# Performance work log

Measured on AMD Instinct MI355X. Metric: run time of the kernel, lower is better.

The kernel has to match this reference:

```python
import jax, jax.numpy as jnp
import numpy as np

B, L, D_MODEL = 4, 2048, 1024
N_HEADS, FEAT, HEAD_DIM = 16, 16, 64
CHUNK = 128
EPS = 1e-12


def taylor_exp(x):
    """2nd-order Taylor feature map of exp(q.k/sqrt(d)).
    x: (b, h, l, f) -> (b, h, l, 1 + f + f*f)"""
    f = x.shape[-1]
    r2 = jnp.sqrt(jnp.asarray(2.0, x.dtype))
    rd = jnp.sqrt(jnp.asarray(float(f), x.dtype))      # sqrt(d)
    rrd = jnp.sqrt(rd)                                  # d**0.25
    x2 = (x[..., :, None] * x[..., None, :]).reshape(*x.shape[:-1], f * f) / r2
    ones = jnp.ones_like(x[..., :1])
    return jnp.concatenate([ones, x / rrd, x2 / rd], axis=-1)


def setup_inputs() -> dict:
    key = jax.random.key(0)
    k1, k2, k3, k4, k5 = jax.random.split(key, 5)
    s = 0.02
    return {
        "hidden_states": jax.random.normal(k1, (B, L, D_MODEL), jnp.float32),
        "Wq": jax.random.normal(k2, (N_HEADS * FEAT, D_MODEL), jnp.float32) * s,
        "Wk": jax.random.normal(k3, (N_HEADS * FEAT, D_MODEL), jnp.float32) * s,
        "Wv": jax.random.normal(k4, (N_HEADS * HEAD_DIM, D_MODEL), jnp.float32) * s,
        "Wo": jax.random.normal(k5, (D_MODEL, N_HEADS * HEAD_DIM), jnp.float32) * s,
    }


def reference(hidden_states, Wq, Wk, Wv, Wo):
    b, l, _ = hidden_states.shape
    # projections (Linear without bias: x @ W.T)
    q = (hidden_states @ Wq.T).reshape(b, l, N_HEADS, FEAT).transpose(0, 2, 1, 3)
    k = (hidden_states @ Wk.T).reshape(b, l, N_HEADS, FEAT).transpose(0, 2, 1, 3)
    v = (hidden_states @ Wv.T).reshape(b, l, N_HEADS, HEAD_DIM).transpose(0, 2, 1, 3)

    qf = taylor_exp(q)  # (b, h, l, De) with De = 1 + f + f^2 = 273
    kf = taylor_exp(k)
    De = qf.shape[-1]

    # chunked causal linear attention: same math as cumulative kv-state
    n = l // CHUNK
    qc = jnp.moveaxis(qf.reshape(b, N_HEADS, n, CHUNK, De), 2, 0)       # (n,b,h,c,De)
    kc = jnp.moveaxis(kf.reshape(b, N_HEADS, n, CHUNK, De), 2, 0)
    vc = jnp.moveaxis(v.reshape(b, N_HEADS, n, CHUNK, HEAD_DIM), 2, 0)
    mask = jnp.tril(jnp.ones((CHUNK, CHUNK), qf.dtype))

    def step(carry, xs):
        S, z = carry                       # S: (b,h,De,e), z: (b,h,De)
        qi, ki, vi = xs
        attn = jnp.einsum('bhid,bhjd->bhij', qi, ki) * mask
        num = jnp.einsum('bhij,bhje->bhie', attn, vi) \
            + jnp.einsum('bhid,bhde->bhie', qi, S)
        den = attn.sum(-1) + jnp.einsum('bhid,bhd->bhi', qi, z)
        yi = num / (den[..., None] + EPS)
        S = S + jnp.einsum('bhjd,bhje->bhde', ki, vi)
        z = z + ki.sum(2)
        return (S, z), yi

    S0 = jnp.zeros((b, N_HEADS, De, HEAD_DIM), qf.dtype)
    z0 = jnp.zeros((b, N_HEADS, De), qf.dtype)
    _, ys = jax.lax.scan(step, (S0, z0), (qc, kc, vc))
    y = jnp.moveaxis(ys, 0, 2).reshape(b, N_HEADS, l, HEAD_DIM)          # (b,h,l,e)
    y = y.transpose(0, 2, 1, 3).reshape(b, l, N_HEADS * HEAD_DIM)        # (b,l,h*e)
    return y @ Wo.T
```

## Files before the change

kernel.cpp:

```cpp
#include <hip/hip_runtime.h>
#include <hip/hip_bf16.h>

#define BB 4
#define LL 2048
#define DM 1024
#define NH 16
#define FEAT 16
#define HD 64
#define CHUNK 128
#define NCHUNK 16
#define NEXT 65
#define SROW 18720
#define EPS 1e-12f
#define INV_R2RD 0.17677669529663688f
#define QKVLD 1536

typedef short bf16x8_t __attribute__((ext_vector_type(8)));
typedef float f32x4_t  __attribute__((ext_vector_type(4)));

__device__ __forceinline__ float b2f(unsigned short u) {
    union { unsigned int i; float f; } x; x.i = ((unsigned int)u) << 16; return x.f;
}
__device__ __forceinline__ unsigned short f2b(float f) {
    __hip_bfloat16 h = __float2bfloat16(f);
    return *reinterpret_cast<unsigned short*>(&h);
}

__global__ __launch_bounds__(256)
void cast_all(const float* __restrict__ hs, const float* __restrict__ wq,
              const float* __restrict__ wk, const float* __restrict__ wv,
              const float* __restrict__ wo, unsigned short* __restrict__ hs_bf,
              unsigned short* __restrict__ wqkv, unsigned short* __restrict__ wo_bf)
{
    const int i = (blockIdx.x * 256 + threadIdx.x) * 4;
    const float* s; unsigned short* d;
    if (i < 8388608)       { s = hs + i;             d = hs_bf + i; }
    else if (i < 8650752)  { s = wq + (i - 8388608); d = wqkv + (i - 8388608); }
    else if (i < 8912896)  { s = wk + (i - 8650752); d = wqkv + 262144 + (i - 8650752); }
    else if (i < 9961472)  { s = wv + (i - 8912896); d = wqkv + 524288 + (i - 8912896); }
    else if (i < 11010048) { s = wo + (i - 9961472); d = wo_bf + (i - 9961472); }
    else return;
    float4 v = *(const float4*)s;
    ushort4 o; o.x = f2b(v.x); o.y = f2b(v.y); o.z = f2b(v.z); o.w = f2b(v.w);
    *(ushort4*)d = o;
}

__global__ __launch_bounds__(512, 2)
void gemm_bf16_192(const unsigned short* __restrict__ A, const unsigned short* __restrict__ Bw,
                   unsigned short* __restrict__ C, int K, int lda, int ldb, int ldc)
{
    __shared__ unsigned short lds[57344];
    const int tid  = threadIdx.x;
    const int wid  = tid >> 6, lane = tid & 63;
    const int wm   = wid >> 2, wn = wid & 3;
    const int ml   = lane & 15, quad = lane >> 4;
    const int nwg = gridDim.x * gridDim.y;
    const int lin = blockIdx.y * gridDim.x + blockIdx.x;
    const int swz_id = (lin & 7) * (nwg >> 3) + (lin >> 3);
    const int m0   = (swz_id / gridDim.x) * 256, n0 = (swz_id % gridDim.x) * 192;
    const int NT   = K >> 6;

    const int srow  = tid >> 3;
    const int scol  = ((tid & 7) ^ (srow & 7)) << 3;
    const int wbase = wid << 9;

    auto stage_unit = [&](int t, int isB, int u) {
        const unsigned short* g0 = isB ? Bw : A;
        const int ld = isB ? ldb : lda;
        const int rb = (isB ? n0 : m0) + u * 64 + srow;
        unsigned short* lb = lds + (isB ? 32768 + (t & 1) * 12288 : ((t & 1) << 14))
                             + (u << 12) + wbase;
        const unsigned short* g = g0 + (size_t)rb * ld + (t << 6) + scol;
        __builtin_amdgcn_global_load_lds((const __attribute__((address_space(1))) void*)g,
                                         (__attribute__((address_space(3))) void*)lb, 16, 0, 0);
    };

    f32x4_t acc[8][3];
#pragma unroll
    for (int i = 0; i < 8; ++i)
#pragma unroll
        for (int j = 0; j < 3; ++j) acc[i][j] = (f32x4_t){0.f, 0.f, 0.f, 0.f};

    stage_unit(0, 0, 0); stage_unit(0, 0, 1); stage_unit(0, 0, 2); stage_unit(0, 0, 3);
    stage_unit(0, 1, 0); stage_unit(0, 1, 1); stage_unit(0, 1, 2);
    stage_unit(1, 0, 0); stage_unit(1, 0, 1);
    stage_unit(1, 1, 0); stage_unit(1, 1, 1);
    stage_unit(1, 0, 2); stage_unit(1, 0, 3);
    asm volatile("s_waitcnt vmcnt(6)" ::: "memory");
    __builtin_amdgcn_s_barrier();

    const int swz  = (ml & 7) << 3;
    const int c0   = (quad << 3) ^ swz;
    const int c1   = (32 + (quad << 3)) ^ swz;
    const int arow = ml << 6;

    bf16x8_t aA[4][2], bLo[2][2], bN2[2];

    for (int t = 0; t < NT; ++t) {
        const int ab = (t & 1) << 14;
        const int bb = 32768 + (t & 1) * 12288;

#pragma unroll
        for (int m = 0; m < 4; ++m) {
            const int r = ab + ((2 * m + wm) << 10) + arow;
            aA[m][0] = *(const bf16x8_t*)&lds[r + c0];
            aA[m][1] = *(const bf16x8_t*)&lds[r + c1];
        }
#pragma unroll
        for (int n = 0; n < 2; ++n) {
            const int r = bb + (wn * 48 + n * 16 + ml) * 64;
            bLo[n][0] = *(const bf16x8_t*)&lds[r + c0];
            bLo[n][1] = *(const bf16x8_t*)&lds[r + c1];
        }
        if (t + 1 < NT) stage_unit(t + 1, 1, 2);
        __builtin_amdgcn_s_barrier();
        asm volatile("s_waitcnt lgkmcnt(0)" ::: "memory");
        __builtin_amdgcn_sched_barrier(0);
        __builtin_amdgcn_s_setprio(1);
#pragma unroll
        for (int m = 0; m < 4; ++m)
#pragma unroll
            for (int n = 0; n < 2; ++n) {
                acc[m][n] = __builtin_amdgcn_mfma_f32_16x16x32_bf16(aA[m][0], bLo[n][0], acc[m][n], 0, 0, 0);
                acc[m][n] = __builtin_amdgcn_mfma_f32_16x16x32_bf16(aA[m][1], bLo[n][1], acc[m][n], 0, 0, 0);
            }
        __builtin_amdgcn_s_setprio(0);
        __builtin_amdgcn_s_barrier();

        {
            const int r = bb + (wn * 48 + 32 + ml) * 64;
            bN2[0] = *(const bf16x8_t*)&lds[r + c0];
            bN2[1] = *(const bf16x8_t*)&lds[r + c1];
        }
        if (t + 2 < NT) { stage_unit(t + 2, 0, 0); stage_unit(t + 2, 0, 1); }
        __builtin_amdgcn_s_barrier();
        asm volatile("s_waitcnt lgkmcnt(0)" ::: "memory");
        __builtin_amdgcn_sched_barrier(0);
        __builtin_amdgcn_s_setprio(1);
#pragma unroll
        for (int m = 0; m < 4; ++m) {
            acc[m][2] = __builtin_amdgcn_mfma_f32_16x16x32_bf16(aA[m][0], bN2[0], acc[m][2], 0, 0, 0);
            acc[m][2] = __builtin_amdgcn_mfma_f32_16x16x32_bf16(aA[m][1], bN2[1], acc[m][2], 0, 0, 0);
        }
        __builtin_amdgcn_s_setprio(0);
        __builtin_amdgcn_s_barrier();

#pragma unroll
        for (int m = 0; m < 4; ++m) {
            const int r = ab + ((2 * (m + 4) + wm) << 10) + arow;
            aA[m][0] = *(const bf16x8_t*)&lds[r + c0];
            aA[m][1] = *(const bf16x8_t*)&lds[r + c1];
        }
        if (t + 2 < NT) { stage_unit(t + 2, 1, 0); stage_unit(t + 2, 1, 1); }
        __builtin_amdgcn_s_barrier();
        asm volatile("s_waitcnt lgkmcnt(0)" ::: "memory");
        __builtin_amdgcn_sched_barrier(0);
        __builtin_amdgcn_s_setprio(1);
#pragma unroll
        for (int m = 0; m < 4; ++m)
#pragma unroll
            for (int n = 0; n < 2; ++n) {
                acc[4 + m][n] = __builtin_amdgcn_mfma_f32_16x16x32_bf16(aA[m][0], bLo[n][0], acc[4 + m][n], 0, 0, 0);
                acc[4 + m][n] = __builtin_amdgcn_mfma_f32_16x16x32_bf16(aA[m][1], bLo[n][1], acc[4 + m][n], 0, 0, 0);
            }
        __builtin_amdgcn_s_setprio(0);
        __builtin_amdgcn_s_barrier();

        if (t + 2 < NT) { stage_unit(t + 2, 0, 2); stage_unit(t + 2, 0, 3); }
        __builtin_amdgcn_s_barrier();
        asm volatile("s_waitcnt lgkmcnt(0)" ::: "memory");
        __builtin_amdgcn_sched_barrier(0);
        __builtin_amdgcn_s_setprio(1);
#pragma unroll
        for (int m = 0; m < 4; ++m) {
            acc[4 + m][2] = __builtin_amdgcn_mfma_f32_16x16x32_bf16(aA[m][0], bN2[0], acc[4 + m][2], 0, 0, 0);
            acc[4 + m][2] = __builtin_amdgcn_mfma_f32_16x16x32_bf16(aA[m][1], bN2[1], acc[4 + m][2], 0, 0, 0);
        }
        __builtin_amdgcn_s_setprio(0);
        if (t + 2 < NT)      asm volatile("s_waitcnt vmcnt(6)" ::: "memory");
        else if (t + 1 < NT) asm volatile("s_waitcnt vmcnt(0)" ::: "memory");
        __builtin_amdgcn_s_barrier();
    }

#pragma unroll
    for (int m = 0; m < 8; ++m) {
        const int rbase = m0 + (2 * m + wm) * 16 + quad * 4;
#pragma unroll
        for (int n = 0; n < 3; ++n) {
            const int col = n0 + wn * 48 + n * 16 + ml;
#pragma unroll
            for (int r = 0; r < 4; ++r)
                C[(size_t)(rbase + r) * ldc + col] = f2b(acc[m][n][r]);
        }
    }
}

__global__ __launch_bounds__(512, 2)
void gemm_bf16_128x256(const unsigned short* __restrict__ A, const unsigned short* __restrict__ Bw,
                       float* __restrict__ C, int K, int lda, int ldb, int ldc)
{
    __shared__ unsigned short lds[49152];
    const int tid  = threadIdx.x;
    const int wid  = tid >> 6, lane = tid & 63;
    const int wm   = wid >> 2, wn = wid & 3;
    const int ml   = lane & 15, quad = lane >> 4;
    const int nwg = gridDim.x * gridDim.y;
    const int lin = blockIdx.y * gridDim.x + blockIdx.x;
    const int swz_id = (lin & 7) * (nwg >> 3) + (lin >> 3);
    const int m0   = (swz_id / gridDim.x) * 128, n0 = (swz_id % gridDim.x) * 256;
    const int NT   = K >> 6;

    const int srow  = tid >> 3;
    const int scol  = ((tid & 7) ^ (srow & 7)) << 3;
    const int wbase = wid << 9;

    auto stage_unit = [&](int t, int isB, int u) {
        const unsigned short* g0 = isB ? Bw : A;
        const int ld = isB ? ldb : lda;
        const int rb = (isB ? n0 : m0) + u * 64 + srow;
        const int k0 = t << 6;
        unsigned short* lb = lds + (isB ? 16384 : 0) + ((t & 1) << (isB ? 14 : 13))
                             + (u << 12) + wbase;
        const unsigned short* g = g0 + (size_t)rb * ld + k0 + scol;
        __builtin_amdgcn_global_load_lds((const __attribute__((address_space(1))) void*)g,
                                         (__attribute__((address_space(3))) void*)lb, 16, 0, 0);
    };

    f32x4_t acc[4][4];
#pragma unroll
    for (int i = 0; i < 4; ++i)
#pragma unroll
        for (int j = 0; j < 4; ++j) acc[i][j] = (f32x4_t){0.f, 0.f, 0.f, 0.f};

    stage_unit(0, 0, 0); stage_unit(0, 0, 1);
    stage_unit(0, 1, 0); stage_unit(0, 1, 1); stage_unit(0, 1, 2); stage_unit(0, 1, 3);
    stage_unit(1, 0, 0); stage_unit(1, 0, 1);
    stage_unit(1, 1, 0); stage_unit(1, 1, 1);
    asm volatile("s_waitcnt vmcnt(4)" ::: "memory");
    __builtin_amdgcn_s_barrier();

    const int swz  = (ml & 7) << 3;
    const int c0   = (quad << 3) ^ swz;
    const int c1   = (32 + (quad << 3)) ^ swz;
    const int arow = ml << 6;

    bf16x8_t aA[4][2], bF[2][2];

    for (int t = 0; t < NT; ++t) {
        const int ab = (t & 1) << 13;
        const int bb = 16384 + ((t & 1) << 14);

#pragma unroll
        for (int m = 0; m < 4; ++m) {
            const int r = ab + ((2 * m + wm) << 10) + arow;
            aA[m][0] = *(const bf16x8_t*)&lds[r + c0];
            aA[m][1] = *(const bf16x8_t*)&lds[r + c1];
        }
#pragma unroll
        for (int n = 0; n < 2; ++n) {
            const int r = bb + ((4 * n + wn) << 10) + arow;
            bF[n][0] = *(const bf16x8_t*)&lds[r + c0];
            bF[n][1] = *(const bf16x8_t*)&lds[r + c1];
        }
        if (t + 1 < NT) { stage_unit(t + 1, 1, 2); stage_unit(t + 1, 1, 3); }
        __builtin_amdgcn_s_barrier();
        asm volatile("s_waitcnt lgkmcnt(0)" ::: "memory");
        __builtin_amdgcn_sched_barrier(0);
        __builtin_amdgcn_s_setprio(1);
#pragma unroll
        for (int m = 0; m < 4; ++m)
#pragma unroll
            for (int n = 0; n < 2; ++n) {
                acc[m][n] = __builtin_amdgcn_mfma_f32_16x16x32_bf16(aA[m][0], bF[n][0], acc[m][n], 0, 0, 0);
                acc[m][n] = __builtin_amdgcn_mfma_f32_16x16x32_bf16(aA[m][1], bF[n][1], acc[m][n], 0, 0, 0);
            }
        __builtin_amdgcn_s_setprio(0);
        __builtin_amdgcn_s_barrier();

#pragma unroll
        for (int n = 0; n < 2; ++n) {
            const int r = bb + ((4 * (n + 2) + wn) << 10) + arow;
            bF[n][0] = *(const bf16x8_t*)&lds[r + c0];
            bF[n][1] = *(const bf16x8_t*)&lds[r + c1];
        }
        if (t + 2 < NT) {
            stage_unit(t + 2, 0, 0); stage_unit(t + 2, 0, 1);
            stage_unit(t + 2, 1, 0); stage_unit(t + 2, 1, 1);
        }
        __builtin_amdgcn_s_barrier();
        asm volatile("s_waitcnt lgkmcnt(0)" ::: "memory");
        __builtin_amdgcn_sched_barrier(0);
        __builtin_amdgcn_s_setprio(1);
#pragma unroll
        for (int m = 0; m < 4; ++m)
#pragma unroll
            for (int n = 0; n < 2; ++n) {
                acc[m][2 + n] = __builtin_amdgcn_mfma_f32_16x16x32_bf16(aA[m][0], bF[n][0], acc[m][2 + n], 0, 0, 0);
                acc[m][2 + n] = __builtin_amdgcn_mfma_f32_16x16x32_bf16(aA[m][1], bF[n][1], acc[m][2 + n], 0, 0, 0);
            }
        __builtin_amdgcn_s_setprio(0);
        if (t + 2 < NT)      asm volatile("s_waitcnt vmcnt(4)" ::: "memory");
        else if (t + 1 < NT) asm volatile("s_waitcnt vmcnt(0)" ::: "memory");
        __builtin_amdgcn_s_barrier();
    }

#pragma unroll
    for (int m = 0; m < 4; ++m) {
        const int rbase = m0 + (2 * m + wm) * 16 + quad * 4;
#pragma unroll
        for (int n = 0; n < 4; ++n) {
            const int col = n0 + (4 * n + wn) * 16 + ml;
#pragma unroll
            for (int r = 0; r < 4; ++r)
                C[(size_t)(rbase + r) * ldc + col] = acc[m][n][r];
        }
    }
}

__global__ __launch_bounds__(256)
void state_scan(const unsigned short* __restrict__ qkv, unsigned short* __restrict__ STg)
{
    __shared__ unsigned short KT[16 * 136];
    __shared__ unsigned short VT[80 * 136];

    const int g  = blockIdx.x & 3, bh = blockIdx.x >> 2;
    const int b = bh >> 4, h = bh & 15;
    const int tid = threadIdx.x;
    const int wave = tid >> 6, lane = tid & 63;
    const int ml = lane & 15, kg8 = (lane >> 4) * 8, quad4 = (lane >> 4) * 4;
    const int mtA = g + 4 * wave;
    const bool hasB = (wave == 0) && (g < 2);
    const int mtB = 16 + g;

    const int row = tid >> 1, half = tid & 1;
    const unsigned short* src = qkv + (size_t)(b * LL) * QKVLD;

    if (half == 0) {
        VT[64 * 136 + row] = 0x3F80;
    } else {
#pragma unroll
        for (int e = 65; e < 80; ++e) VT[e * 136 + row] = 0;
    }

    uint4 kvn, vvn[4];
    {
        const size_t rg = (size_t)row * QKVLD;
        kvn = *(const uint4*)(src + rg + 256 + h * 16 + half * 8);
#pragma unroll
        for (int cc = 0; cc < 4; ++cc)
            vvn[cc] = *(const uint4*)(src + rg + 512 + h * 64 + half * 32 + cc * 8);
    }

    f32x4_t prefA[5], prefB[5];
#pragma unroll
    for (int nt = 0; nt < 5; ++nt) {
        prefA[nt] = (f32x4_t){0.f, 0.f, 0.f, 0.f};
        prefB[nt] = (f32x4_t){0.f, 0.f, 0.f, 0.f};
    }

    auto do_tile = [&](int mt, f32x4_t* pref, size_t Sb) {
        const int d = mt * 16 + ml;
        bf16x8_t af[4];
#pragma unroll
        for (int ks = 0; ks < 4; ++ks) {
            const int jb = ks * 32 + kg8;
            unsigned short o[8];
            if (d >= 24 && d < 280) {
                const int e = d - 24, a = e >> 4, bq = e & 15;
                bf16x8_t ka = *(const bf16x8_t*)&KT[a  * 136 + jb];
                bf16x8_t kb = *(const bf16x8_t*)&KT[bq * 136 + jb];
#pragma unroll
                for (int j = 0; j < 8; ++j)
                    o[j] = f2b(b2f((unsigned short)ka[j]) * b2f((unsigned short)kb[j]) * INV_R2RD);
            } else if (d == 0) {
#pragma unroll
                for (int j = 0; j < 8; ++j) o[j] = 0x3F80;
            } else if (d <= 16) {
                bf16x8_t kx = *(const bf16x8_t*)&KT[(d - 1) * 136 + jb];
#pragma unroll
                for (int j = 0; j < 8; ++j) o[j] = f2b(b2f((unsigned short)kx[j]) * 0.5f);
            } else {
#pragma unroll
                for (int j = 0; j < 8; ++j) o[j] = 0;
            }
            af[ks] = *(const bf16x8_t*)o;
        }
        bf16x8_t bfr[5][4];
#pragma unroll
        for (int nt = 0; nt < 5; ++nt)
#pragma unroll
            for (int ks = 0; ks < 4; ++ks)
                bfr[nt][ks] = *(const bf16x8_t*)&VT[(nt * 16 + ml) * 136 + ks * 32 + kg8];
#pragma unroll
        for (int nt = 0; nt < 5; ++nt) {
            ushort4 pk;
            pk.x = f2b(pref[nt][0]); pk.y = f2b(pref[nt][1]);
            pk.z = f2b(pref[nt][2]); pk.w = f2b(pref[nt][3]);
            if (nt < 4) {
                *(ushort4*)(STg + Sb + (size_t)mt * 1040 + (nt * 16 + ml) * 16 + quad4) = pk;
            } else if (ml == 0) {
                *(ushort4*)(STg + Sb + (size_t)mt * 1040 + 1024 + quad4) = pk;
            }
        }
        __builtin_amdgcn_s_setprio(1);
#pragma unroll
        for (int nt = 0; nt < 5; ++nt)
#pragma unroll
            for (int ks = 0; ks < 4; ++ks)
                pref[nt] = __builtin_amdgcn_mfma_f32_16x16x32_bf16(af[ks], bfr[nt][ks], pref[nt], 0, 0, 0);
        __builtin_amdgcn_s_setprio(0);
    };

    for (int c = 0; c < NCHUNK; ++c) {
        {
            const unsigned short* kp = (const unsigned short*)&kvn;
#pragma unroll
            for (int i = 0; i < 8; ++i) KT[(half * 8 + i) * 136 + row] = kp[i];
#pragma unroll
            for (int cc = 0; cc < 4; ++cc) {
                const unsigned short* vp = (const unsigned short*)&vvn[cc];
#pragma unroll
                for (int i = 0; i < 8; ++i) VT[(half * 32 + cc * 8 + i) * 136 + row] = vp[i];
            }
        }
        __syncthreads();
        if (c + 1 < NCHUNK) {
            const size_t rg = (size_t)((c + 1) * CHUNK + row) * QKVLD;
            kvn = *(const uint4*)(src + rg + 256 + h * 16 + half * 8);
#pragma unroll
            for (int cc = 0; cc < 4; ++cc)
                vvn[cc] = *(const uint4*)(src + rg + 512 + h * 64 + half * 32 + cc * 8);
        }

        const size_t Sb = (size_t)(bh * NCHUNK + c) * SROW;
        do_tile(mtA, prefA, Sb);
        if (hasB) do_tile(mtB, prefB, Sb);
        __syncthreads();
    }
}

#define OFF_VT 0
#define OFF_QP 0
#define OFF_KP 5120
#define OFF_A  10880

__global__ __launch_bounds__(256)
void out_kernel(const unsigned short* __restrict__ qkv_ro, const unsigned short* __restrict__ STg,
                unsigned short* __restrict__ qkv_w)
{
    __shared__ unsigned short smem[28288];

    const int x = blockIdx.x;
    const int c = x & 15, bh = x >> 4;
    const int b = bh >> 4, h = bh & 15;
    const int tid = threadIdx.x;
    const int w = tid >> 6, lane = tid & 63;
    const int ml = lane & 15, quad = lane >> 4, kg8 = quad * 8;
    const size_t rowbase = (size_t)(b * LL + c * CHUNK);
    const size_t Sbase = (size_t)x * SROW;

    const unsigned short* stp = STg + Sbase + (size_t)(quad >> 1) * 1040 + (quad & 1) * 8;
    bf16x8_t stf[3][5];
    auto ldst = [&](int kq, int slot) {
#pragma unroll
        for (int nt = 0; nt < 5; ++nt)
            stf[slot][nt] = *(const bf16x8_t*)(stp + (size_t)kq * 2080 + (nt * 16 + ml) * 16);
    };

    const int row = tid >> 1, half = tid & 1;
    uint4 qv = *(const uint4*)(qkv_ro + (rowbase + row) * QKVLD + h * 16 + half * 8);
    uint4 kv = *(const uint4*)(qkv_ro + (rowbase + row) * QKVLD + 256 + h * 16 + half * 8);
    uint4 vreg[4];
#pragma unroll
    for (int cc = 0; cc < 4; ++cc)
        vreg[cc] = *(const uint4*)(qkv_ro + (rowbase + row) * QKVLD + 512 + h * 64 + half * 32 + cc * 8);
    ldst(0, 0);
    ldst(1, 1);

    *(uint4*)&smem[OFF_QP + row * 40 + half * 8] = qv;
    *(uint4*)&smem[OFF_QP + row * 40 + 16 + half * 8] = (uint4){0, 0, 0, 0};
    *(uint4*)&smem[OFF_KP + row * 40 + half * 8] = kv;
    *(uint4*)&smem[OFF_KP + row * 40 + 16 + half * 8] = (uint4){0, 0, 0, 0};
    __syncthreads();

    {
        bf16x8_t q0 = *(const bf16x8_t*)&smem[OFF_QP + (w * 32 + ml) * 40 + kg8];
        bf16x8_t q1 = *(const bf16x8_t*)&smem[OFF_QP + (w * 32 + 16 + ml) * 40 + kg8];
#pragma unroll
        for (int nt = 0; nt < 8; ++nt) {
            bf16x8_t kf = *(const bf16x8_t*)&smem[OFF_KP + (nt * 16 + ml) * 40 + kg8];
            f32x4_t a0 = __builtin_amdgcn_mfma_f32_16x16x32_bf16(q0, kf, (f32x4_t){0,0,0,0}, 0, 0, 0);
            f32x4_t a1 = __builtin_amdgcn_mfma_f32_16x16x32_bf16(q1, kf, (f32x4_t){0,0,0,0}, 0, 0, 0);
            const int j = nt * 16 + ml;
#pragma unroll
            for (int r = 0; r < 4; ++r) {
                int i0 = w * 32 + quad * 4 + r;
                float s0 = a0[r] * 0.25f;
                float v0 = (j <= i0) ? (1.f + s0 + 0.5f * s0 * s0) : 0.f;
                smem[OFF_A + i0 * 136 + j] = f2b(v0);
                int i1 = i0 + 16;
                float s1 = a1[r] * 0.25f;
                float v1 = (j <= i1) ? (1.f + s1 + 0.5f * s1 * s1) : 0.f;
                smem[OFF_A + i1 * 136 + j] = f2b(v1);
            }
        }
    }
    const int r0 = w * 32 + ml, r1 = r0 + 16;
    float qA[16], qB[16];
    {
        bf16x8_t t0 = *(const bf16x8_t*)&smem[OFF_QP + r0 * 40];
        bf16x8_t t1 = *(const bf16x8_t*)&smem[OFF_QP + r0 * 40 + 8];
        bf16x8_t t2 = *(const bf16x8_t*)&smem[OFF_QP + r1 * 40];
        bf16x8_t t3 = *(const bf16x8_t*)&smem[OFF_QP + r1 * 40 + 8];
#pragma unroll
        for (int i = 0; i < 8; ++i) {
            qA[i] = b2f((unsigned short)t0[i]); qA[8 + i] = b2f((unsigned short)t1[i]);
            qB[i] = b2f((unsigned short)t2[i]); qB[8 + i] = b2f((unsigned short)t3[i]);
        }
    }
    float qselA[8], qselB[8];
#pragma unroll
    for (int j = 0; j < 8; ++j) {
        qselA[j] = (quad & 1) ? qA[j] : qA[8 + j];
        qselB[j] = (quad & 1) ? qB[j] : qB[8 + j];
    }
    __syncthreads();

    {
#pragma unroll
        for (int cc = 0; cc < 4; ++cc) {
            const unsigned short* vp = (const unsigned short*)&vreg[cc];
#pragma unroll
            for (int i = 0; i < 8; ++i) smem[OFF_VT + (half * 32 + cc * 8 + i) * 136 + row] = vp[i];
        }
        if (half == 0) {
            smem[OFF_VT + 64 * 136 + row] = 0x3F80;
        } else {
#pragma unroll
            for (int e = 65; e < 80; ++e) smem[OFF_VT + e * 136 + row] = 0;
        }
    }
    __syncthreads();

    f32x4_t acc[2][5];
#pragma unroll
    for (int mt = 0; mt < 2; ++mt)
#pragma unroll
        for (int nt = 0; nt < 5; ++nt) acc[mt][nt] = (f32x4_t){0.f, 0.f, 0.f, 0.f};

    ldst(2, 2);

#pragma unroll
    for (int ks = 0; ks < 4; ++ks) {
        bf16x8_t af0 = *(const bf16x8_t*)&smem[OFF_A + (w * 32 + ml) * 136 + ks * 32 + kg8];
        bf16x8_t af1 = *(const bf16x8_t*)&smem[OFF_A + (w * 32 + 16 + ml) * 136 + ks * 32 + kg8];
        __builtin_amdgcn_s_setprio(1);
#pragma unroll
        for (int nt = 0; nt < 5; ++nt) {
            bf16x8_t bv = *(const bf16x8_t*)&smem[OFF_VT + (nt * 16 + ml) * 136 + ks * 32 + kg8];
            acc[0][nt] = __builtin_amdgcn_mfma_f32_16x16x32_bf16(af0, bv, acc[0][nt], 0, 0, 0);
            acc[1][nt] = __builtin_amdgcn_mfma_f32_16x16x32_bf16(af1, bv, acc[1][nt], 0, 0, 0);
        }
        __builtin_amdgcn_s_setprio(0);
    }

#pragma unroll
    for (int kq = 0; kq < 9; ++kq) {
        bf16x8_t qf[2];
#pragma unroll
        for (int mt = 0; mt < 2; ++mt) {
            const float* q    = (mt == 0) ? qA : qB;
            const float* qsel = (mt == 0) ? qselA : qselB;
            const int d0 = kq * 32 + kg8;
            unsigned short o[8];
            if (d0 >= 24 && d0 < 280) {
                const int i2 = 2 * kq;
                const float base = (quad == 3) ? q[i2 > 15 ? 15 : i2]
                                 : (quad == 0) ? q[i2 < 2 ? 0 : i2 - 2]
                                               : q[i2 < 1 ? 0 : i2 - 1];
                const float qa = base * INV_R2RD;
#pragma unroll
                for (int j = 0; j < 8; ++j) o[j] = f2b(qa * qsel[j]);
            } else if (d0 == 0) {
                o[0] = 0x3F80;
#pragma unroll
                for (int j = 1; j < 8; ++j) o[j] = f2b(q[j - 1] * 0.5f);
            } else if (d0 == 8) {
#pragma unroll
                for (int j = 0; j < 8; ++j) o[j] = f2b(q[7 + j] * 0.5f);
            } else if (d0 == 16) {
                o[0] = f2b(q[15] * 0.5f);
#pragma unroll
                for (int j = 1; j < 8; ++j) o[j] = 0;
            } else {
#pragma unroll
                for (int j = 0; j < 8; ++j) o[j] = 0;
            }
            qf[mt] = *(const bf16x8_t*)o;
        }
        __builtin_amdgcn_s_setprio(1);
#pragma unroll
        for (int nt = 0; nt < 5; ++nt) {
            acc[0][nt] = __builtin_amdgcn_mfma_f32_16x16x32_bf16(qf[0], stf[kq % 3][nt], acc[0][nt], 0, 0, 0);
            acc[1][nt] = __builtin_amdgcn_mfma_f32_16x16x32_bf16(qf[1], stf[kq % 3][nt], acc[1][nt], 0, 0, 0);
        }
        __builtin_amdgcn_s_setprio(0);
        if (kq + 3 < 9) ldst(kq + 3, kq % 3);
    }

#pragma unroll
    for (int mt = 0; mt < 2; ++mt) {
        float den[4];
#pragma unroll
        for (int r = 0; r < 4; ++r) den[r] = __shfl(acc[mt][4][r], lane & 48);
#pragma unroll
        for (int r = 0; r < 4; ++r) {
            const size_t grow = rowbase + w * 32 + mt * 16 + quad * 4 + r;
            const float rc = 1.f / (den[r] + EPS);
#pragma unroll
            for (int nt = 0; nt < 4; ++nt)
                qkv_w[grow * QKVLD + 512 + h * 64 + nt * 16 + ml] = f2b(acc[mt][nt][r] * rc);
        }
    }
}

extern "C" void kernel_launch(void* const* d_in, const int* in_sizes, int n_in,
                              void* d_out, int out_size, void* d_ws, size_t ws_size,
                              hipStream_t stream)
{
    (void)in_sizes; (void)n_in; (void)out_size; (void)ws_size;
    const float* hs = (const float*)d_in[0];
    const float* Wq = (const float*)d_in[1];
    const float* Wk = (const float*)d_in[2];
    const float* Wv = (const float*)d_in[3];
    const float* Wo = (const float*)d_in[4];
    float* out = (float*)d_out;

    char* ws = (char*)d_ws;
    unsigned short* STg   = (unsigned short*)ws;
    unsigned short* hs_bf = (unsigned short*)ws;
    size_t off = 47185920;
    unsigned short* qkv   = (unsigned short*)(ws + off); off += 25165824;
    unsigned short* Wqkv  = (unsigned short*)(ws + off); off += 3145728;
    unsigned short* Wo_bf = (unsigned short*)(ws + off); off += 2097152;

    cast_all<<<10752, 256, 0, stream>>>(hs, Wq, Wk, Wv, Wo, hs_bf, Wqkv, Wo_bf);
    gemm_bf16_192<<<dim3(8, 32), 512, 0, stream>>>(hs_bf, Wqkv, qkv,
                                                   DM, DM, DM, QKVLD);
    state_scan<<<256, 256, 0, stream>>>(qkv, STg);
    out_kernel<<<1024, 256, 0, stream>>>(qkv, STg, qkv);
    gemm_bf16_128x256<<<dim3(4, 64), 512, 0, stream>>>(qkv + 512, Wo_bf, out,
                                                       DM, QKVLD, DM, DM);
}
```

Measured before the change: 202.8 us.

## Split serial state scan into parallel per-chunk state kernel plus prefix-sum pass

The sequential per-(batch,head) chunk loop that accumulated the KV state in registers is replaced by a kernel computing each chunk's local K^T V state independently (1024 blocks instead of 256), followed by a separate exclusive prefix-sum kernel over chunks in global memory. LDS row pitch changes from 136 to 152 and the V/K transposes into shared memory use vectorized ushort4 stores. This trades more parallelism for an extra global read/write pass over the state buffer and an extra launch. The prefix sums now accumulate per-chunk states after bf16 rounding rather than the fp32 running sum, which changes numerics slightly.

```diff
diff --git a/kernel.cpp b/kernel.cpp
--- a/kernel.cpp
+++ b/kernel.cpp
@@ -14,6 +14,7 @@
 #define EPS 1e-12f
 #define INV_R2RD 0.17677669529663688f
 #define QKVLD 1536
+#define LP 152
 
 typedef short bf16x8_t __attribute__((ext_vector_type(8)));
 typedef float f32x4_t  __attribute__((ext_vector_type(4)));
@@ -318,47 +319,69 @@
 }
 
 __global__ __launch_bounds__(256)
-void state_scan(const unsigned short* __restrict__ qkv, unsigned short* __restrict__ STg)
+void state_kernel(const unsigned short* __restrict__ qkv, unsigned short* __restrict__ STg)
 {
-    __shared__ unsigned short KT[16 * 136];
-    __shared__ unsigned short VT[80 * 136];
-
-    const int g  = blockIdx.x & 3, bh = blockIdx.x >> 2;
+    __shared__ unsigned short KT[16 * LP];
+    __shared__ unsigned short VT[80 * LP];
+
+    const int x = blockIdx.x;
+    const int c = x & 15, bh = x >> 4;
     const int b = bh >> 4, h = bh & 15;
     const int tid = threadIdx.x;
     const int wave = tid >> 6, lane = tid & 63;
-    const int ml = lane & 15, kg8 = (lane >> 4) * 8, quad4 = (lane >> 4) * 4;
-    const int mtA = g + 4 * wave;
-    const bool hasB = (wave == 0) && (g < 2);
-    const int mtB = 16 + g;
-
-    const int row = tid >> 1, half = tid & 1;
-    const unsigned short* src = qkv + (size_t)(b * LL) * QKVLD;
-
-    if (half == 0) {
-        VT[64 * 136 + row] = 0x3F80;
-    } else {
-#pragma unroll
-        for (int e = 65; e < 80; ++e) VT[e * 136 + row] = 0;
-    }
-
-    uint4 kvn, vvn[4];
+    const int ml = lane & 15, kg8 = (lane >> 4) * 8;
+    const int quad4 = (lane >> 4) * 4;
+    const size_t rowbase = (size_t)(b * LL + c * CHUNK);
+    const size_t Sbase = (size_t)x * SROW;
+
     {
-        const size_t rg = (size_t)row * QKVLD;
-        kvn = *(const uint4*)(src + rg + 256 + h * 16 + half * 8);
-#pragma unroll
-        for (int cc = 0; cc < 4; ++cc)
-            vvn[cc] = *(const uint4*)(src + rg + 512 + h * 64 + half * 32 + cc * 8);
-    }
-
-    f32x4_t prefA[5], prefB[5];
-#pragma unroll
-    for (int nt = 0; nt < 5; ++nt) {
-        prefA[nt] = (f32x4_t){0.f, 0.f, 0.f, 0.f};
-        prefB[nt] = (f32x4_t){0.f, 0.f, 0.f, 0.f};
-    }
-
-    auto do_tile = [&](int mt, f32x4_t* pref, size_t Sb) {
+        const int rg = tid & 31, eb = tid >> 5;
+        uint4 vv[4];
+#pragma unroll
+        for (int i = 0; i < 4; ++i)
+            vv[i] = *(const uint4*)(qkv + (rowbase + 4 * rg + i) * QKVLD + 512 + h * 64 + eb * 8);
+        const unsigned short* p0 = (const unsigned short*)&vv[0];
+        const unsigned short* p1 = (const unsigned short*)&vv[1];
+        const unsigned short* p2 = (const unsigned short*)&vv[2];
+        const unsigned short* p3 = (const unsigned short*)&vv[3];
+#pragma unroll
+        for (int e = 0; e < 8; ++e) {
+            ushort4 w4; w4.x = p0[e]; w4.y = p1[e]; w4.z = p2[e]; w4.w = p3[e];
+            *(ushort4*)&VT[(eb * 8 + e) * LP + 4 * rg] = w4;
+        }
+        if (eb < 2) {
+            uint4 kv4[4];
+#pragma unroll
+            for (int i = 0; i < 4; ++i)
+                kv4[i] = *(const uint4*)(qkv + (rowbase + 4 * rg + i) * QKVLD + 256 + h * 16 + eb * 8);
+            const unsigned short* k0 = (const unsigned short*)&kv4[0];
+            const unsigned short* k1 = (const unsigned short*)&kv4[1];
+            const unsigned short* k2 = (const unsigned short*)&kv4[2];
+            const unsigned short* k3 = (const unsigned short*)&kv4[3];
+#pragma unroll
+            for (int e = 0; e < 8; ++e) {
+                ushort4 w4; w4.x = k0[e]; w4.y = k1[e]; w4.z = k2[e]; w4.w = k3[e];
+                *(ushort4*)&KT[(eb * 8 + e) * LP + 4 * rg] = w4;
+            }
+        }
+        const int row = tid >> 1, half = tid & 1;
+        if (half == 0) {
+            VT[64 * LP + row] = 0x3F80;
+        } else {
+#pragma unroll
+            for (int e = 65; e < 80; ++e) VT[e * LP + row] = 0;
+        }
+    }
+    __syncthreads();
+
+    bf16x8_t bfr[5][4];
+#pragma unroll
+    for (int nt = 0; nt < 5; ++nt)
+#pragma unroll
+        for (int ks = 0; ks < 4; ++ks)
+            bfr[nt][ks] = *(const bf16x8_t*)&VT[(nt * 16 + ml) * LP + ks * 32 + kg8];
+
+    for (int mt = wave; mt < 18; mt += 4) {
         const int d = mt * 16 + ml;
         bf16x8_t af[4];
 #pragma unroll
@@ -367,8 +390,8 @@
             unsigned short o[8];
             if (d >= 24 && d < 280) {
                 const int e = d - 24, a = e >> 4, bq = e & 15;
-                bf16x8_t ka = *(const bf16x8_t*)&KT[a  * 136 + jb];
-                bf16x8_t kb = *(const bf16x8_t*)&KT[bq * 136 + jb];
+                bf16x8_t ka = *(const bf16x8_t*)&KT[a  * LP + jb];
+                bf16x8_t kb = *(const bf16x8_t*)&KT[bq * LP + jb];
 #pragma unroll
                 for (int j = 0; j < 8; ++j)
                     o[j] = f2b(b2f((unsigned short)ka[j]) * b2f((unsigned short)kb[j]) * INV_R2RD);
@@ -376,7 +399,7 @@
 #pragma unroll
                 for (int j = 0; j < 8; ++j) o[j] = 0x3F80;
             } else if (d <= 16) {
-                bf16x8_t kx = *(const bf16x8_t*)&KT[(d - 1) * 136 + jb];
+                bf16x8_t kx = *(const bf16x8_t*)&KT[(d - 1) * LP + jb];
 #pragma unroll
                 for (int j = 0; j < 8; ++j) o[j] = f2b(b2f((unsigned short)kx[j]) * 0.5f);
             } else {
@@ -385,70 +408,62 @@
             }
             af[ks] = *(const bf16x8_t*)o;
         }
-        bf16x8_t bfr[5][4];
+        f32x4_t acc[5];
+#pragma unroll
+        for (int nt = 0; nt < 5; ++nt) acc[nt] = (f32x4_t){0.f, 0.f, 0.f, 0.f};
+        __builtin_amdgcn_s_setprio(1);
 #pragma unroll
         for (int nt = 0; nt < 5; ++nt)
 #pragma unroll
             for (int ks = 0; ks < 4; ++ks)
-                bfr[nt][ks] = *(const bf16x8_t*)&VT[(nt * 16 + ml) * 136 + ks * 32 + kg8];
+                acc[nt] = __builtin_amdgcn_mfma_f32_16x16x32_bf16(af[ks], bfr[nt][ks], acc[nt], 0, 0, 0);
+        __builtin_amdgcn_s_setprio(0);
 #pragma unroll
         for (int nt = 0; nt < 5; ++nt) {
             ushort4 pk;
-            pk.x = f2b(pref[nt][0]); pk.y = f2b(pref[nt][1]);
-            pk.z = f2b(pref[nt][2]); pk.w = f2b(pref[nt][3]);
+            pk.x = f2b(acc[nt][0]); pk.y = f2b(acc[nt][1]);
+            pk.z = f2b(acc[nt][2]); pk.w = f2b(acc[nt][3]);
             if (nt < 4) {
-                *(ushort4*)(STg + Sb + (size_t)mt * 1040 + (nt * 16 + ml) * 16 + quad4) = pk;
+                *(ushort4*)(STg + Sbase + (size_t)mt * 1040 + (nt * 16 + ml) * 16 + quad4) = pk;
             } else if (ml == 0) {
-                *(ushort4*)(STg + Sb + (size_t)mt * 1040 + 1024 + quad4) = pk;
-            }
-        }
-        __builtin_amdgcn_s_setprio(1);
-#pragma unroll
-        for (int nt = 0; nt < 5; ++nt)
-#pragma unroll
-            for (int ks = 0; ks < 4; ++ks)
-                pref[nt] = __builtin_amdgcn_mfma_f32_16x16x32_bf16(af[ks], bfr[nt][ks], pref[nt], 0, 0, 0);
-        __builtin_amdgcn_s_setprio(0);
-    };
-
+                *(ushort4*)(STg + Sbase + (size_t)mt * 1040 + 1024 + quad4) = pk;
+            }
+        }
+    }
+}
+
+__global__ __launch_bounds__(256)
+void scan_S(unsigned short* __restrict__ STg) {
+    const int bh  = blockIdx.y;
+    const int idx = blockIdx.x * 256 + threadIdx.x;
+    if (idx >= SROW / 8) return;
+    const size_t base = (size_t)bh * NCHUNK * SROW + (size_t)idx * 8;
+    uint4 v[NCHUNK];
+#pragma unroll
+    for (int c = 0; c < NCHUNK; ++c)
+        v[c] = *(const uint4*)(STg + base + (size_t)c * SROW);
+    float acc[8] = {};
+#pragma unroll
     for (int c = 0; c < NCHUNK; ++c) {
-        {
-            const unsigned short* kp = (const unsigned short*)&kvn;
-#pragma unroll
-            for (int i = 0; i < 8; ++i) KT[(half * 8 + i) * 136 + row] = kp[i];
-#pragma unroll
-            for (int cc = 0; cc < 4; ++cc) {
-                const unsigned short* vp = (const unsigned short*)&vvn[cc];
-#pragma unroll
-                for (int i = 0; i < 8; ++i) VT[(half * 32 + cc * 8 + i) * 136 + row] = vp[i];
-            }
-        }
-        __syncthreads();
-        if (c + 1 < NCHUNK) {
-            const size_t rg = (size_t)((c + 1) * CHUNK + row) * QKVLD;
-            kvn = *(const uint4*)(src + rg + 256 + h * 16 + half * 8);
-#pragma unroll
-            for (int cc = 0; cc < 4; ++cc)
-                vvn[cc] = *(const uint4*)(src + rg + 512 + h * 64 + half * 32 + cc * 8);
-        }
-
-        const size_t Sb = (size_t)(bh * NCHUNK + c) * SROW;
-        do_tile(mtA, prefA, Sb);
-        if (hasB) do_tile(mtB, prefB, Sb);
-        __syncthreads();
+        const unsigned short* vp = (const unsigned short*)&v[c];
+        uint4 o;
+        unsigned short* op = (unsigned short*)&o;
+#pragma unroll
+        for (int i = 0; i < 8; ++i) { op[i] = f2b(acc[i]); acc[i] += b2f(vp[i]); }
+        *(uint4*)(STg + base + (size_t)c * SROW) = o;
     }
 }
 
 #define OFF_VT 0
 #define OFF_QP 0
 #define OFF_KP 5120
-#define OFF_A  10880
+#define OFF_A  12160
 
 __global__ __launch_bounds__(256)
 void out_kernel(const unsigned short* __restrict__ qkv_ro, const unsigned short* __restrict__ STg,
                 unsigned short* __restrict__ qkv_w)
 {
-    __shared__ unsigned short smem[28288];
+    __shared__ unsigned short smem[31616];
 
     const int x = blockIdx.x;
     const int c = x & 15, bh = x >> 4;
@@ -468,12 +483,13 @@
     };
 
     const int row = tid >> 1, half = tid & 1;
+    const int rg = tid & 31, eb = tid >> 5;
     uint4 qv = *(const uint4*)(qkv_ro + (rowbase + row) * QKVLD + h * 16 + half * 8);
     uint4 kv = *(const uint4*)(qkv_ro + (rowbase + row) * QKVLD + 256 + h * 16 + half * 8);
     uint4 vreg[4];
 #pragma unroll
-    for (int cc = 0; cc < 4; ++cc)
-        vreg[cc] = *(const uint4*)(qkv_ro + (rowbase + row) * QKVLD + 512 + h * 64 + half * 32 + cc * 8);
+    for (int i = 0; i < 4; ++i)
+        vreg[i] = *(const uint4*)(qkv_ro + (rowbase + 4 * rg + i) * QKVLD + 512 + h * 64 + eb * 8);
     ldst(0, 0);
     ldst(1, 1);
 
@@ -497,11 +513,11 @@
                 int i0 = w * 32 + quad * 4 + r;
                 float s0 = a0[r] * 0.25f;
                 float v0 = (j <= i0) ? (1.f + s0 + 0.5f * s0 * s0) : 0.f;
-                smem[OFF_A + i0 * 136 + j] = f2b(v0);
+                smem[OFF_A + i0 * LP + j] = f2b(v0);
                 int i1 = i0 + 16;
                 float s1 = a1[r] * 0.25f;
                 float v1 = (j <= i1) ? (1.f + s1 + 0.5f * s1 * s1) : 0.f;
-                smem[OFF_A + i1 * 136 + j] = f2b(v1);
+                smem[OFF_A + i1 * LP + j] = f2b(v1);
             }
         }
     }
@@ -527,17 +543,20 @@
     __syncthreads();
 
     {
-#pragma unroll
-        for (int cc = 0; cc < 4; ++cc) {
-            const unsigned short* vp = (const unsigned short*)&vreg[cc];
-#pragma unroll
-            for (int i = 0; i < 8; ++i) smem[OFF_VT + (half * 32 + cc * 8 + i) * 136 + row] = vp[i];
+        const unsigned short* p0 = (const unsigned short*)&vreg[0];
+        const unsigned short* p1 = (const unsigned short*)&vreg[1];
+        const unsigned short* p2 = (const unsigned short*)&vreg[2];
+        const unsigned short* p3 = (const unsigned short*)&vreg[3];
+#pragma unroll
+        for (int e = 0; e < 8; ++e) {
+            ushort4 w4; w4.x = p0[e]; w4.y = p1[e]; w4.z = p2[e]; w4.w = p3[e];
+            *(ushort4*)&smem[OFF_VT + (eb * 8 + e) * LP + 4 * rg] = w4;
         }
         if (half == 0) {
-            smem[OFF_VT + 64 * 136 + row] = 0x3F80;
+            smem[OFF_VT + 64 * LP + row] = 0x3F80;
         } else {
 #pragma unroll
-            for (int e = 65; e < 80; ++e) smem[OFF_VT + e * 136 + row] = 0;
+            for (int e = 65; e < 80; ++e) smem[OFF_VT + e * LP + row] = 0;
         }
     }
     __syncthreads();
@@ -552,12 +571,12 @@
 
 #pragma unroll
     for (int ks = 0; ks < 4; ++ks) {
-        bf16x8_t af0 = *(const bf16x8_t*)&smem[OFF_A + (w * 32 + ml) * 136 + ks * 32 + kg8];
-        bf16x8_t af1 = *(const bf16x8_t*)&smem[OFF_A + (w * 32 + 16 + ml) * 136 + ks * 32 + kg8];
+        bf16x8_t af0 = *(const bf16x8_t*)&smem[OFF_A + (w * 32 + ml) * LP + ks * 32 + kg8];
+        bf16x8_t af1 = *(const bf16x8_t*)&smem[OFF_A + (w * 32 + 16 + ml) * LP + ks * 32 + kg8];
         __builtin_amdgcn_s_setprio(1);
 #pragma unroll
         for (int nt = 0; nt < 5; ++nt) {
-            bf16x8_t bv = *(const bf16x8_t*)&smem[OFF_VT + (nt * 16 + ml) * 136 + ks * 32 + kg8];
+            bf16x8_t bv = *(const bf16x8_t*)&smem[OFF_VT + (nt * 16 + ml) * LP + ks * 32 + kg8];
             acc[0][nt] = __builtin_amdgcn_mfma_f32_16x16x32_bf16(af0, bv, acc[0][nt], 0, 0, 0);
             acc[1][nt] = __builtin_amdgcn_mfma_f32_16x16x32_bf16(af1, bv, acc[1][nt], 0, 0, 0);
         }
@@ -647,7 +666,8 @@
     cast_all<<<10752, 256, 0, stream>>>(hs, Wq, Wk, Wv, Wo, hs_bf, Wqkv, Wo_bf);
     gemm_bf16_192<<<dim3(8, 32), 512, 0, stream>>>(hs_bf, Wqkv, qkv,
                                                    DM, DM, DM, QKVLD);
-    state_scan<<<256, 256, 0, stream>>>(qkv, STg);
+    state_kernel<<<1024, 256, 0, stream>>>(qkv, STg);
+    scan_S<<<dim3(10, 64), 256, 0, stream>>>(STg);
     out_kernel<<<1024, 256, 0, stream>>>(qkv, STg, qkv);
     gemm_bf16_128x256<<<dim3(4, 64), 512, 0, stream>>>(qkv + 512, Wo_bf, out,
                                                        DM, QKVLD, DM, DM);
```

Result: faster. 194.2 us (-4.2%).
